# Optimization experiments

Hardware: AMD Instinct MI355X
Metric: run time of the kernel (lower is better)

The kernel has to match this reference:

```python
import jax, jax.numpy as jnp
import numpy as np

PAD = 4
KERNEL = 1
MAX_DISP = 4
STRIDE1 = 1
STRIDE2 = 1


def setup_inputs() -> dict:
    key = jax.random.key(0)
    k1, k2 = jax.random.split(key)
    B, C, H, W = 16, 128, 96, 160
    input1 = jax.random.normal(k1, (B, C, H, W), dtype=jnp.float32)
    input2 = jax.random.normal(k2, (B, C, H, W), dtype=jnp.float32)
    return {"input1": input1, "input2": input2}


def _correlation(input1, input2):
    # FlowNet-style patch cross-correlation (corr_multiply=1).
    # Output[b, d, y, x] = sum_{c, patch} I1[b,c,patch(y,x)] * I2[b,c,patch(y+dy,x+dx)] / (K*K*C)
    B, C, H, W = input1.shape
    kr = (KERNEL - 1) // 2  # kernel radius (0 for KERNEL=1)
    p1 = jnp.pad(input1, ((0, 0), (0, 0), (PAD, PAD), (PAD, PAD)))
    p2 = jnp.pad(input2, ((0, 0), (0, 0), (PAD, PAD), (PAD, PAD)))
    norm = jnp.float32(KERNEL * KERNEL * C)
    outs = []
    for dy in range(-MAX_DISP, MAX_DISP + 1, STRIDE2):
        for dx in range(-MAX_DISP, MAX_DISP + 1, STRIDE2):
            acc = jnp.zeros((B, H, W), dtype=input1.dtype)
            for ki in range(-kr, kr + 1):
                for kj in range(-kr, kr + 1):
                    a = p1[:, :, PAD + ki:PAD + ki + H, PAD + kj:PAD + kj + W]
                    b = p2[:, :, PAD + ki + dy:PAD + ki + dy + H,
                              PAD + kj + dx:PAD + kj + dx + W]
                    acc = acc + jnp.sum(a * b, axis=1)
            outs.append(acc / norm)
    return jnp.stack(outs, axis=1)  # [B, (2*md/s2+1)^2, H, W]


def reference(input1, input2):
    return _correlation(input1, input2)
```

## Files before the change

### kernel.cpp

```cpp
#include <hip/hip_runtime.h>
#include <stdint.h>

typedef __bf16 bf16;
typedef __attribute__((ext_vector_type(4))) __bf16 bf16x4;
typedef __attribute__((ext_vector_type(8))) __bf16 bf16x8;
typedef __attribute__((ext_vector_type(4))) float f32x4;
typedef __attribute__((ext_vector_type(4))) unsigned int u32x4;

#define W_ 160
#define H_ 96
#define C_ 128
#define B_ 16
#define HW_ (H_ * W_)
#define NXT 10
#define NYB8 12
#define NBLK (B_ * NYB8 * NXT)
#define SLICEB 10240
#define YB 40960
#define ROWSB 1536
#define CHB (16 * ROWSB)
#define WSSTR 1312

__device__ float g_zero[16];

__device__ __forceinline__ void g2l16(const void* g, void* l) {
    __builtin_amdgcn_global_load_lds(
        (const __attribute__((address_space(1))) void*)g,
        (__attribute__((address_space(3))) void*)l, 16, 0, 0);
}

__global__ __launch_bounds__(256) void t2_kernel(const float* __restrict__ in2,
                                                 char* __restrict__ o) {
    __shared__ __align__(16) char T[40960];
    const int L   = blockIdx.x;
    const int tid = threadIdx.x;
    const float* src = in2 + (size_t)(L / H_) * C_ * HW_ + (size_t)(L % H_) * W_;
    char* dst = o + (size_t)L * YB;
    const float SC = 1.0f / 128.0f;
#pragma unroll
    for (int rd = 0; rd < 5; ++rd) {
        const int s  = rd * 256 + tid;
        const int cq = s / 40;
        const int x4 = s - cq * 40;
        const float* p = src + (size_t)(4 * cq) * HW_ + 4 * x4;
        const float4 v0 = *(const float4*)(p);
        const float4 v1 = *(const float4*)(p + HW_);
        const float4 v2 = *(const float4*)(p + 2 * HW_);
        const float4 v3 = *(const float4*)(p + 3 * HW_);
        const int oq = cq >> 1, half = cq & 1;
#pragma unroll
        for (int xj = 0; xj < 4; ++xj) {
            const int x   = 4 * x4 + xj;
            const int pos = oq ^ ((x >> 2) & 15);
            bf16x4 pk;
            pk[0] = (bf16)(((const float*)&v0)[xj] * SC);
            pk[1] = (bf16)(((const float*)&v1)[xj] * SC);
            pk[2] = (bf16)(((const float*)&v2)[xj] * SC);
            pk[3] = (bf16)(((const float*)&v3)[xj] * SC);
            *(bf16x4*)(T + x * 256 + pos * 16 + half * 8) = pk;
        }
    }
    __syncthreads();
#pragma unroll
    for (int wr = 0; wr < 10; ++wr) {
        const int s2  = wr * 256 + tid;
        const int ck  = s2 / 640;
        const int r   = s2 - ck * 640;
        const int x   = r >> 2;
        const int gsw = r & 3;
        const int gg  = gsw ^ ((x >> 1) & 3);
        const int oo  = ck * 4 + gg;
        const int pos = oo ^ ((x >> 2) & 15);
        const u32x4 v = *(const u32x4*)(T + x * 256 + pos * 16);
        *(u32x4*)(dst + (size_t)s2 * 16) = v;
    }
}

__global__ __launch_bounds__(512, 4) void corr_mfma6(const float* __restrict__ in1,
                                                     const char* __restrict__ in2t,
                                                     float* __restrict__ out) {
    __shared__ __align__(16) char Bsm[2 * CHB + 512];

    const int L   = ((int)blockIdx.x & 7) * (NBLK / 8) + ((int)blockIdx.x >> 3);
    const int b   = L / (NYB8 * NXT);
    const int rem = L % (NYB8 * NXT);
    const int yb  = rem / NXT;
    const int xt  = rem % NXT;
    const int x0  = xt * 16, y0 = yb * 8;

    const int tid  = threadIdx.x;
    const int wv   = __builtin_amdgcn_readfirstlane(tid >> 6);
    const int lane = tid & 63;
    const int n    = lane & 15;
    const int g    = lane >> 4;
    const int y    = y0 + wv;

    const char* i2tb = in2t + (size_t)b * (H_ * YB);

    const float* abase = in1 + (size_t)b * C_ * HW_ + (size_t)y * W_ + (x0 + n);
    bf16x8 afrag[4];
#pragma unroll
    for (int ck = 0; ck < 4; ++ck) {
        float ar[8];
#pragma unroll
        for (int j = 0; j < 8; ++j)
            ar[j] = abase[(size_t)(ck * 32 + g * 8 + j) * HW_];
#pragma unroll
        for (int j = 0; j < 8; ++j)
            afrag[ck][j] = (bf16)ar[j];
    }
    asm volatile("s_waitcnt vmcnt(0)" ::: "memory");
    __builtin_amdgcn_sched_barrier(0);

    unsigned soff[3];
    bool     sv[3];
#pragma unroll
    for (int rd = 0; rd < 3; ++rd) {
        const int slot = rd * 512 + tid;
        const int row  = slot / 96;
        const int sl   = slot - row * 96;
        const int gy   = y0 - 4 + row;
        const int x    = x0 - 4 + (sl >> 2);
        sv[rd] = ((unsigned)gy < (unsigned)H_) && ((unsigned)x < (unsigned)W_);
        const int gy_c = min(max(gy, 0), H_ - 1);
        const int ofs  = max((x0 - 4) * 64 + sl * 16, 0);
        soff[rd] = (unsigned)(gy_c * YB + ofs);
    }

    int rboff[2];
#pragma unroll
    for (int t = 0; t < 2; ++t) {
        const int xl = n + 16 * t;
        const int sw = g ^ (((xl + 12) >> 1) & 3);
        rboff[t] = (xl * 4 + sw) * 16;
    }

    f32x4 acc[9][2];
#pragma unroll
    for (int dyi = 0; dyi < 9; ++dyi)
#pragma unroll
        for (int t = 0; t < 2; ++t)
            acc[dyi][t] = (f32x4){0.f, 0.f, 0.f, 0.f};

#define STAGE(CK, DST)                                                        \
    {                                                                         \
        const char* bck = i2tb + (CK) * SLICEB;                               \
        _Pragma("unroll")                                                     \
        for (int rd = 0; rd < 3; ++rd)                                        \
            g2l16(sv[rd] ? (const void*)(bck + soff[rd])                      \
                         : (const void*)g_zero,                               \
                  (void*)((DST) + (rd * 512 + tid) * 16));                    \
    }
#define WAITB(N)                                                              \
    {                                                                         \
        asm volatile("s_waitcnt vmcnt(" #N ")" ::: "memory");                 \
        __builtin_amdgcn_s_barrier();                                         \
        __builtin_amdgcn_sched_barrier(0);                                    \
    }
#define RBAR                                                                  \
    {                                                                         \
        asm volatile("s_waitcnt lgkmcnt(0)" ::: "memory");                    \
        __builtin_amdgcn_s_barrier();                                         \
        __builtin_amdgcn_sched_barrier(0);                                    \
    }
#define COMPUTE(CK, BUF)                                                      \
    {                                                                         \
        _Pragma("unroll")                                                     \
        for (int dyi = 0; dyi < 9; ++dyi) {                                   \
            const int rowoff = (wv + dyi) * ROWSB;                            \
            _Pragma("unroll")                                                 \
            for (int t = 0; t < 2; ++t) {                                     \
                const bf16x8 bfrag =                                          \
                    *(const bf16x8*)((BUF) + rowoff + rboff[t]);              \
                acc[dyi][t] = __builtin_amdgcn_mfma_f32_16x16x32_bf16(        \
                    afrag[CK], bfrag, acc[dyi][t], 0, 0, 0);                  \
            }                                                                 \
        }                                                                     \
    }

    STAGE(0, Bsm);
    STAGE(1, Bsm + CHB);
    WAITB(3);
    COMPUTE(0, Bsm);
    RBAR;
    STAGE(2, Bsm);
    WAITB(3);
    COMPUTE(1, Bsm + CHB);
    RBAR;
    STAGE(3, Bsm + CHB);
    WAITB(3);
    COMPUTE(2, Bsm);
    WAITB(0);
    COMPUTE(3, Bsm + CHB);
#undef STAGE
#undef WAITB
#undef RBAR
#undef COMPUTE

    __syncthreads();

    float* wsw = (float*)Bsm + wv * WSSTR;
#pragma unroll
    for (int dyi = 0; dyi < 9; ++dyi)
#pragma unroll
        for (int t = 0; t < 2; ++t)
#pragma unroll
            for (int rr = 0; rr < 4; ++rr) {
                const int m = 4 * g + rr;
                const int d = n + 16 * t - m;
                if ((unsigned)d <= 8u)
                    wsw[(dyi * 9 + d) * 16 + m] = acc[dyi][t][rr];
            }
    __syncthreads();

    const int mm = lane & 15, rg = lane >> 4;
    const size_t ob = (size_t)(b * 81) * HW_ + (size_t)y * W_ + (x0 + mm);
#pragma unroll
    for (int q4 = 0; q4 < 20; ++q4) {
        const int rho = q4 * 4 + rg;
        out[ob + (size_t)rho * HW_] = wsw[rho * 16 + mm];
    }
    if (rg == 0)
        out[ob + (size_t)80 * HW_] = wsw[80 * 16 + mm];
}

extern "C" void kernel_launch(void* const* d_in, const int* in_sizes, int n_in,
                              void* d_out, int out_size, void* d_ws, size_t ws_size,
                              hipStream_t stream) {
    const float* in1 = (const float*)d_in[0];
    const float* in2 = (const float*)d_in[1];
    float* out = (float*)d_out;
    (void)in_sizes; (void)n_in; (void)out_size; (void)ws_size;
    char* in2t = (char*)d_ws;
    hipLaunchKernelGGL(t2_kernel, dim3(B_ * H_), dim3(256), 0, stream, in2, in2t);
    hipLaunchKernelGGL(corr_mfma6, dim3(NBLK), dim3(512), 0, stream, in1, in2t, out);
}
```

Baseline: 101.0 us.

## Triple-buffer B-slice staging and replace zero-fill loads with output masking

```diff
diff --git a/kernel.cpp b/kernel.cpp
--- a/kernel.cpp
+++ b/kernel.cpp
@@ -19,9 +19,8 @@
 #define YB 40960
 #define ROWSB 1536
 #define CHB (16 * ROWSB)
-#define WSSTR 1312
-
-__device__ float g_zero[16];
+#define LDSB (3 * CHB + 512)
+#define WSSTR 1408
 
 __device__ __forceinline__ void g2l16(const void* g, void* l) {
     __builtin_amdgcn_global_load_lds(
@@ -76,10 +75,10 @@
     }
 }
 
-__global__ __launch_bounds__(512, 4) void corr_mfma6(const float* __restrict__ in1,
+__global__ __launch_bounds__(512, 4) void corr_mfma7(const float* __restrict__ in1,
                                                      const char* __restrict__ in2t,
                                                      float* __restrict__ out) {
-    __shared__ __align__(16) char Bsm[2 * CHB + 512];
+    __shared__ __align__(16) char Bsm[LDSB];
 
     const int L   = ((int)blockIdx.x & 7) * (NBLK / 8) + ((int)blockIdx.x >> 3);
     const int b   = L / (NYB8 * NXT);
@@ -113,15 +112,12 @@
     __builtin_amdgcn_sched_barrier(0);
 
     unsigned soff[3];
-    bool     sv[3];
 #pragma unroll
     for (int rd = 0; rd < 3; ++rd) {
         const int slot = rd * 512 + tid;
         const int row  = slot / 96;
         const int sl   = slot - row * 96;
         const int gy   = y0 - 4 + row;
-        const int x    = x0 - 4 + (sl >> 2);
-        sv[rd] = ((unsigned)gy < (unsigned)H_) && ((unsigned)x < (unsigned)W_);
         const int gy_c = min(max(gy, 0), H_ - 1);
         const int ofs  = max((x0 - 4) * 64 + sl * 16, 0);
         soff[rd] = (unsigned)(gy_c * YB + ofs);
@@ -147,8 +143,7 @@
         const char* bck = i2tb + (CK) * SLICEB;                               \
         _Pragma("unroll")                                                     \
         for (int rd = 0; rd < 3; ++rd)                                        \
-            g2l16(sv[rd] ? (const void*)(bck + soff[rd])                      \
-                         : (const void*)g_zero,                               \
+            g2l16((const void*)(bck + soff[rd]),                              \
                   (void*)((DST) + (rd * 512 + tid) * 16));                    \
     }
 #define WAITB(N)                                                              \
@@ -180,18 +175,17 @@
 
     STAGE(0, Bsm);
     STAGE(1, Bsm + CHB);
-    WAITB(3);
+    STAGE(2, Bsm + 2 * CHB);
+    WAITB(6);
     COMPUTE(0, Bsm);
     RBAR;
-    STAGE(2, Bsm);
+    STAGE(3, Bsm);
+    WAITB(6);
+    COMPUTE(1, Bsm + CHB);
     WAITB(3);
-    COMPUTE(1, Bsm + CHB);
-    RBAR;
-    STAGE(3, Bsm + CHB);
-    WAITB(3);
-    COMPUTE(2, Bsm);
+    COMPUTE(2, Bsm + 2 * CHB);
     WAITB(0);
-    COMPUTE(3, Bsm + CHB);
+    COMPUTE(3, Bsm);
 #undef STAGE
 #undef WAITB
 #undef RBAR
@@ -199,6 +193,15 @@
 
     __syncthreads();
 
+    float xv[2];
+#pragma unroll
+    for (int t = 0; t < 2; ++t)
+        xv[t] = ((unsigned)(x0 - 4 + n + 16 * t) < (unsigned)W_) ? 1.f : 0.f;
+    float yv[9];
+#pragma unroll
+    for (int dyi = 0; dyi < 9; ++dyi)
+        yv[dyi] = ((unsigned)(y - 4 + dyi) < (unsigned)H_) ? 1.f : 0.f;
+
     float* wsw = (float*)Bsm + wv * WSSTR;
 #pragma unroll
     for (int dyi = 0; dyi < 9; ++dyi)
@@ -209,19 +212,18 @@
                 const int m = 4 * g + rr;
                 const int d = n + 16 * t - m;
                 if ((unsigned)d <= 8u)
-                    wsw[(dyi * 9 + d) * 16 + m] = acc[dyi][t][rr];
+                    wsw[(dyi * 9 + d) * 17 + m] = acc[dyi][t][rr] * xv[t] * yv[dyi];
             }
-    __syncthreads();
 
     const int mm = lane & 15, rg = lane >> 4;
     const size_t ob = (size_t)(b * 81) * HW_ + (size_t)y * W_ + (x0 + mm);
 #pragma unroll
     for (int q4 = 0; q4 < 20; ++q4) {
         const int rho = q4 * 4 + rg;
-        out[ob + (size_t)rho * HW_] = wsw[rho * 16 + mm];
+        out[ob + (size_t)rho * HW_] = wsw[rho * 17 + mm];
     }
     if (rg == 0)
-        out[ob + (size_t)80 * HW_] = wsw[80 * 16 + mm];
+        out[ob + (size_t)80 * HW_] = wsw[80 * 17 + mm];
 }
 
 extern "C" void kernel_launch(void* const* d_in, const int* in_sizes, int n_in,
@@ -233,5 +235,5 @@
     (void)in_sizes; (void)n_in; (void)out_size; (void)ws_size;
     char* in2t = (char*)d_ws;
     hipLaunchKernelGGL(t2_kernel, dim3(B_ * H_), dim3(256), 0, stream, in2, in2t);
-    hipLaunchKernelGGL(corr_mfma6, dim3(NBLK), dim3(512), 0, stream, in1, in2t, out);
-}
+    hipLaunchKernelGGL(corr_mfma7, dim3(NBLK), dim3(512), 0, stream, in1, in2t, out);
+}
```

After: 101.0 us. About the same (-0.0%).
